# Kernel tuning notes

Measured on AMD Instinct MI355X. Metric: run time of the kernel, lower is better.

Reference implementation:

```python
import jax, jax.numpy as jnp
import numpy as np

# ---- config (mirrors DVE_loss.__init__ defaults used here) ----
POW = 0.5
TEMPERATURE = 1.0
SINK_TAU = 0.3      # sink_tau[1]
SINK_ITERS = 30     # sink_iters[1]
LAMBDA_LC = 1.0
SCALE = 20.0        # F.normalize(...) * 20
EPS = 1e-12


def _l2norm(x, axis):
    n = jnp.sqrt(jnp.sum(x * x, axis=axis, keepdims=True))
    return x / jnp.maximum(n, EPS)


def _sinkhorn(log_alpha, tau, n_iters):
    # log-space Sinkhorn normalization (gumbel_sinkhorn with n_samples=1, no noise)
    la = log_alpha / tau
    def body(i, la):
        la = la - jax.nn.logsumexp(la, axis=1, keepdims=True)  # row normalize
        la = la - jax.nn.logsumexp(la, axis=0, keepdims=True)  # col normalize
        return la
    la = jax.lax.fori_loop(0, n_iters, body, la)
    return jnp.exp(la)


def _per_sample(f1, f2, fa, x1):
    # f1, f2, fa: [N, C] (already normalized * 20); x1: [N, 3]
    N = f1.shape[0]
    dt = f1.dtype

    corr_1a = (f1 @ fa.T) / TEMPERATURE                # [N, N]
    smcorr_1a = jax.nn.softmax(corr_1a, axis=1)
    f1_via_fa_t = smcorr_1a @ fa                        # [N, C] (broadcast-weighted sum)
    corr_1a2 = (f1_via_fa_t @ f2.T) / TEMPERATURE       # [N, N]
    smcorr_1a2 = jax.nn.softmax(corr_1a2, axis=1)

    # no-grad sinkhorn target
    sink = jax.lax.stop_gradient(_sinkhorn(corr_1a2, SINK_TAU, SINK_ITERS))

    # pairwise distance matrix (no-grad): ||xi - xj||^pow
    sq = jnp.sum(x1 * x1, axis=-1)                      # [N]
    d2 = jnp.maximum(sq[:, None] + sq[None, :] - 2.0 * (x1 @ x1.T), 0.0)
    dist = jax.lax.stop_gradient(jnp.sqrt(d2) ** POW)   # [N, N]

    smcorr_12 = jax.nn.softmax((f1 @ f2.T) / TEMPERATURE, axis=1)

    L = dist * smcorr_1a2 + dist * smcorr_12
    loss_b = jnp.sum(L) / N

    perm_to_I_b = 3.0 * jnp.sum(jnp.abs(jnp.eye(N, dtype=dt) - sink)) / N
    Lc_b = 3.0 * jnp.sum(jnp.abs(sink - smcorr_1a2)) / N

    # feature_reconstruction(f1, f1) diagnostic (no-grad)
    g = jax.lax.stop_gradient(f1 @ f1.T)                # [N, N]
    smg = jax.nn.softmax(g / TEMPERATURE, axis=1)
    fv = smg @ jax.lax.stop_gradient(f1)                # [N, C] == (f1 @ smcorr.T).T
    corr2 = fv @ jax.lax.stop_gradient(f1).T            # [N, N] (no temperature div)
    sm2 = jax.nn.softmax(corr2, axis=1)
    d_b = -jnp.sum(jnp.diagonal(sm2)) / N

    match_b = jnp.sum(
        (jnp.argmax(smcorr_1a2, axis=1) == jnp.arange(N)).astype(dt))
    return loss_b, Lc_b, perm_to_I_b, d_b, match_b


def setup_inputs() -> dict:
    key = jax.random.key(0)
    k1, k2 = jax.random.split(key)
    feats = jax.random.normal(k1, (16, 2048, 128), dtype=jnp.float32)
    pc0 = jax.random.normal(k2, (8, 2048, 3), dtype=jnp.float32)
    return {"feats": feats, "pc0": pc0, "epoch": 10}


def reference(feats, pc0, epoch):
    x1 = pc0[..., :3]
    feats1 = feats[0::2]                                # [B, N, C]
    feats2 = feats[1::2]
    B = feats1.shape[0]

    f1 = _l2norm(feats1, axis=-1) * SCALE               # normalize per point
    f2 = _l2norm(feats2, axis=-1) * SCALE
    fa = jnp.roll(f1, -1, axis=0)                       # feats1[(b+1) % B]

    loss_b, Lc_b, perm_b, d_b, match_b = jax.vmap(_per_sample)(f1, f2, fa, x1)

    loss = jnp.sum(loss_b)
    Lc = jnp.sum(Lc_b)
    perm_to_I = jnp.sum(perm_b)
    diff_via_recon = jnp.sum(d_b)
    correct_match = jnp.sum(match_b)

    total_loss = loss + LAMBDA_LC * Lc
    return (total_loss / B, loss / B, Lc / B, perm_to_I / B,
            correct_match / B, diff_via_recon / B)
```

## Files before the change

kernel.cpp:

```cpp
#include <hip/hip_runtime.h>
#include <math.h>

constexpr int B_ = 8;
constexpr int N_ = 2048;
constexpr int D_ = 128;
constexpr long long NDl = (long long)N_ * D_;
constexpr long long NNl = (long long)N_ * N_;
constexpr float INV_TAU = 1.0f / 0.3f;
constexpr float SCALE_ = 20.0f;
constexpr float EPS_ = 1e-12f;

typedef __attribute__((ext_vector_type(8))) short short8;
typedef __attribute__((ext_vector_type(4))) float f32x4;
#define MFMA_BF16 __builtin_amdgcn_mfma_f32_16x16x32_bf16

constexpr size_t FL_F  = (size_t)B_ * NDl;
constexpr size_t FL_NN = (size_t)B_ * NNl;
constexpr size_t FL_V  = (size_t)B_ * N_;

constexpr size_t OFF_SQ   = 0;
constexpr size_t OFF_ROWM = OFF_SQ   + FL_V;
constexpr size_t OFF_ROWZ = OFF_ROWM + FL_V;
constexpr size_t OFF_U0   = OFF_ROWZ + FL_V;
constexpr size_t OFF_V0   = OFF_U0   + FL_V;
constexpr size_t OFF_DIAG = OFF_V0   + FL_V;
constexpr size_t OFF_AV   = OFF_DIAG + FL_V;
constexpr size_t OFF_BV   = OFF_AV   + FL_V;
constexpr size_t OFF_ACC  = OFF_BV   + FL_V;
constexpr size_t OFF_PM   = OFF_ACC  + 16;
constexpr size_t OFF_PS   = OFF_PM   + 32 * FL_V;
constexpr size_t OFF_PT   = OFF_PS   + 32 * FL_V;
constexpr size_t OFF_CP   = OFF_PM;
constexpr size_t OFF_PCM  = OFF_PT;
constexpr size_t OFF_PCS  = OFF_PT + 16 * FL_V;
constexpr size_t OFF_C    = OFF_PM + 128 * FL_V;
constexpr size_t OFF_K    = OFF_C  + FL_NN;
constexpr size_t OFF_BF   = OFF_K  + FL_NN / 2;

__device__ inline float bf2f(unsigned int lo16) {
  return __uint_as_float(lo16 << 16);
}
__device__ inline unsigned int f2bf(float x) {
  unsigned int u = __float_as_uint(x);
  u += 0x7fffu + ((u >> 16) & 1u);
  return (u >> 16) & 0xffffu;
}

__global__ __launch_bounds__(64) void k_norm(const float* __restrict__ feats,
                                             unsigned short* __restrict__ f1hi,
                                             unsigned short* __restrict__ f1lo,
                                             unsigned short* __restrict__ f2hi,
                                             unsigned short* __restrict__ f2lo) {
  int r = blockIdx.x, b = blockIdx.y, which = blockIdx.z;
  const float* src = feats + ((size_t)(2 * b + which)) * NDl + (size_t)r * D_;
  int t = threadIdx.x;
  float2 x = *(const float2*)(src + 2 * t);
  float ss = x.x * x.x + x.y * x.y;
#pragma unroll
  for (int off = 32; off; off >>= 1) ss += __shfl_down(ss, off);
  ss = __shfl(ss, 0);
  float s = SCALE_ / fmaxf(sqrtf(ss), EPS_);
  float y0 = x.x * s, y1 = x.y * s;
  unsigned int h0 = f2bf(y0), h1 = f2bf(y1);
  unsigned int l0 = f2bf(y0 - bf2f(h0)), l1 = f2bf(y1 - bf2f(h1));
  size_t o = (size_t)b * NDl + (size_t)r * D_ + 2 * t;
  unsigned short* hb = (which ? f2hi : f1hi);
  unsigned short* lb = (which ? f2lo : f1lo);
  *(unsigned int*)(hb + o) = h0 | (h1 << 16);
  *(unsigned int*)(lb + o) = l0 | (l1 << 16);
}

__global__ __launch_bounds__(256) void k_transpose(const unsigned short* __restrict__ hi,
                                                   const unsigned short* __restrict__ lo,
                                                   unsigned short* __restrict__ thi,
                                                   unsigned short* __restrict__ tlo) {
  __shared__ unsigned short tile[64][66];
  int rt = blockIdx.x, dt = blockIdx.y, z = blockIdx.z;
  int b = z >> 1;
  const unsigned short* s = ((z & 1) ? lo : hi) + (size_t)b * NDl;
  unsigned short* d = ((z & 1) ? tlo : thi) + (size_t)b * NDl;
  int t = threadIdx.x;
  int r = t >> 2, c0 = (t & 3) * 16;
#pragma unroll
  for (int h = 0; h < 2; ++h) {
    uint4 v = *(const uint4*)(s + (size_t)(rt * 64 + r) * D_ + dt * 64 + c0 + h * 8);
    unsigned short* p = &tile[r][c0 + h * 8];
    p[0] = (unsigned short)v.x; p[1] = (unsigned short)(v.x >> 16);
    p[2] = (unsigned short)v.y; p[3] = (unsigned short)(v.y >> 16);
    p[4] = (unsigned short)v.z; p[5] = (unsigned short)(v.z >> 16);
    p[6] = (unsigned short)v.w; p[7] = (unsigned short)(v.w >> 16);
  }
  __syncthreads();
  int dd = t >> 2, r0 = (t & 3) * 16;
#pragma unroll
  for (int h = 0; h < 2; ++h) {
    unsigned int q[4];
#pragma unroll
    for (int e = 0; e < 4; ++e) {
      unsigned short a0 = tile[r0 + h * 8 + 2 * e][dd];
      unsigned short a1 = tile[r0 + h * 8 + 2 * e + 1][dd];
      q[e] = (unsigned int)a0 | ((unsigned int)a1 << 16);
    }
    uint4 v; v.x = q[0]; v.y = q[1]; v.z = q[2]; v.w = q[3];
    *(uint4*)(d + (size_t)(dt * 64 + dd) * N_ + rt * 64 + r0 + h * 8) = v;
  }
}

__global__ __launch_bounds__(256) void k_sq(const float* __restrict__ pc0,
                                            float* __restrict__ sq) {
  int i = blockIdx.x * 256 + threadIdx.x;
  if (i < B_ * N_) {
    float x = pc0[3 * i], y = pc0[3 * i + 1], z = pc0[3 * i + 2];
    sq[i] = x * x + y * y + z * z;
  }
}

template<bool WRITEC, bool TAU, bool SD, bool DIAG>
__global__ __launch_bounds__(256, 2) void k_mm(
    const unsigned short* __restrict__ Ahi_g, const unsigned short* __restrict__ Alo_g,
    const unsigned short* __restrict__ Bhi_g, const unsigned short* __restrict__ Blo_g,
    float* __restrict__ Cb, int roll,
    float* __restrict__ pms, float* __restrict__ pss, float* __restrict__ pts,
    float* __restrict__ diagb,
    const float* __restrict__ pc0, const float* __restrict__ sqv) {
  int bm = blockIdx.x, bn = blockIdx.y, z = blockIdx.z;
  int zb = (z + roll) & 7;
  const unsigned short* A_hi = Ahi_g + (size_t)z * NDl;
  const unsigned short* A_lo = Alo_g + (size_t)z * NDl;
  const unsigned short* B_hi = Bhi_g + (size_t)zb * NDl;
  const unsigned short* B_lo = Blo_g + (size_t)zb * NDl;
  float* C = Cb + (size_t)z * NNl;

  __shared__ __align__(16) unsigned short sAh[128 * 64], sAl[128 * 64];
  __shared__ __align__(16) unsigned short sBh[128 * 64], sBl[128 * 64];
  __shared__ float rpx[128], rpy[128], rpz[128], rps[128];
  __shared__ float cqx[128], cqy[128], cqz[128], cqs[128];

  int t = threadIdx.x;
  int lane = t & 63, w = t >> 6;
  int wm = w >> 1, wn = w & 1;

  if constexpr (SD) {
    const float* xb = pc0 + (size_t)z * N_ * 3;
    const float* sb = sqv + (size_t)z * N_;
    if (t < 128) {
      int r = bm * 128 + t;
      rpx[t] = xb[3 * r]; rpy[t] = xb[3 * r + 1]; rpz[t] = xb[3 * r + 2]; rps[t] = sb[r];
    } else {
      int c = bn * 128 + (t - 128);
      cqx[t - 128] = xb[3 * c]; cqy[t - 128] = xb[3 * c + 1]; cqz[t - 128] = xb[3 * c + 2];
      cqs[t - 128] = sb[c];
    }
  }

  f32x4 acc[4][4] = {};

  for (int kc = 0; kc < D_; kc += 64) {
    if (kc) __syncthreads();
#pragma unroll
    for (int i = 0; i < 4; ++i) {
      int li = i * 256 + t;
      int r = li >> 3;
      int kb = (li & 7) * 16;
      int sidx = (r * 128 + (kb ^ ((r & 7) << 4))) >> 1;
      size_t ga = (size_t)(bm * 128 + r) * D_ + kc + (kb >> 1);
      size_t gb = (size_t)(bn * 128 + r) * D_ + kc + (kb >> 1);
      *(uint4*)(&sAh[sidx]) = *(const uint4*)(A_hi + ga);
      *(uint4*)(&sAl[sidx]) = *(const uint4*)(A_lo + ga);
      *(uint4*)(&sBh[sidx]) = *(const uint4*)(B_hi + gb);
      *(uint4*)(&sBl[sidx]) = *(const uint4*)(B_lo + gb);
    }
    __syncthreads();

    short8 ah[4][2], al[4][2];
#pragma unroll
    for (int m = 0; m < 4; ++m)
#pragma unroll
      for (int ks = 0; ks < 2; ++ks) {
        int row = wm * 64 + m * 16 + (lane & 15);
        int kb = ks * 64 + ((lane >> 4) * 16);
        int idx = (row * 128 + (kb ^ ((row & 7) << 4))) >> 1;
        ah[m][ks] = *(const short8*)(&sAh[idx]);
        al[m][ks] = *(const short8*)(&sAl[idx]);
      }
#pragma unroll
    for (int n = 0; n < 4; ++n) {
#pragma unroll
      for (int ks = 0; ks < 2; ++ks) {
        int row = wn * 64 + n * 16 + (lane & 15);
        int kb = ks * 64 + ((lane >> 4) * 16);
        int idx = (row * 128 + (kb ^ ((row & 7) << 4))) >> 1;
        short8 bh = *(const short8*)(&sBh[idx]);
        short8 bl = *(const short8*)(&sBl[idx]);
#pragma unroll
        for (int m = 0; m < 4; ++m) {
          acc[m][n] = MFMA_BF16(ah[m][ks], bh, acc[m][n], 0, 0, 0);
          acc[m][n] = MFMA_BF16(ah[m][ks], bl, acc[m][n], 0, 0, 0);
          acc[m][n] = MFMA_BF16(al[m][ks], bh, acc[m][n], 0, 0, 0);
        }
      }
    }
  }

  int lrow = (lane >> 4) * 4;
  int lcol = lane & 15;

  if constexpr (WRITEC) {
#pragma unroll
    for (int m = 0; m < 4; ++m) {
      int gr0 = bm * 128 + wm * 64 + m * 16 + lrow;
#pragma unroll
      for (int n = 0; n < 4; ++n) {
        int gc = bn * 128 + wn * 64 + n * 16 + lcol;
        float* Cp = C + (size_t)gr0 * N_ + gc;
#pragma unroll
        for (int rg = 0; rg < 4; ++rg)
          Cp[(size_t)rg * N_] = acc[m][n][rg];
      }
    }
  }

#pragma unroll
  for (int m = 0; m < 4; ++m) {
#pragma unroll
    for (int rg = 0; rg < 4; ++rg) {
      int rib = wm * 64 + m * 16 + lrow + rg;
      float v0 = acc[m][0][rg], v1 = acc[m][1][rg], v2 = acc[m][2][rg], v3 = acc[m][3][rg];
      float mx = fmaxf(fmaxf(v0, v1), fmaxf(v2, v3));
#pragma unroll
      for (int msk = 1; msk < 16; msk <<= 1) mx = fmaxf(mx, __shfl_xor(mx, msk));
      float e0 = __expf(v0 - mx), e1 = __expf(v1 - mx), e2 = __expf(v2 - mx), e3 = __expf(v3 - mx);
      float s = e0 + e1 + e2 + e3;
      float st = 0.f, sd = 0.f;
      if constexpr (TAU)
        st = __expf((v0 - mx) * INV_TAU) + __expf((v1 - mx) * INV_TAU) +
             __expf((v2 - mx) * INV_TAU) + __expf((v3 - mx) * INV_TAU);
      if constexpr (SD) {
        float xi = rpx[rib], yi = rpy[rib], zi = rpz[rib], si = rps[rib];
#pragma unroll
        for (int n = 0; n < 4; ++n) {
          int ci = wn * 64 + n * 16 + lcol;
          float d2 = fmaxf(si + cqs[ci] - 2.f * (xi * cqx[ci] + yi * cqy[ci] + zi * cqz[ci]), 0.f);
          float en = (n == 0) ? e0 : (n == 1) ? e1 : (n == 2) ? e2 : e3;
          sd += en * sqrtf(sqrtf(d2));
        }
      }
#pragma unroll
      for (int msk = 1; msk < 16; msk <<= 1) {
        s += __shfl_xor(s, msk);
        if constexpr (TAU) st += __shfl_xor(st, msk);
        if constexpr (SD) sd += __shfl_xor(sd, msk);
      }
      if (lcol == 0) {
        size_t idx = ((size_t)(z * 32 + bn * 2 + wn)) * N_ + bm * 128 + rib;
        pms[idx] = mx; pss[idx] = s;
        if constexpr (TAU) pts[idx] = st;
        if constexpr (SD) pts[idx] = sd;
      }
    }
  }

  if constexpr (DIAG) {
    if (bm == bn && wm == wn) {
#pragma unroll
      for (int m = 0; m < 4; ++m)
#pragma unroll
        for (int rg = 0; rg < 4; ++rg) {
          int rr = lrow + rg;
          if (lcol == rr)
            diagb[(size_t)z * N_ + bm * 128 + wm * 64 + m * 16 + rr] = acc[m][m][rg];
        }
    }
  }
}

template<bool WMZ, bool TAU, bool SD, bool DIAG, bool MATCH>
__global__ __launch_bounds__(256) void k_comb(const float* __restrict__ pms,
                                              const float* __restrict__ pss,
                                              const float* __restrict__ pts,
                                              const float* __restrict__ diagb,
                                              float* __restrict__ rowm,
                                              float* __restrict__ rowZ,
                                              float* __restrict__ u0,
                                              float* __restrict__ acc) {
  int b = blockIdx.y;
  int r = blockIdx.x * 256 + threadIdx.x;
  float M = -INFINITY, S = 0.f, ST = 0.f, SDa = 0.f;
#pragma unroll
  for (int p = 0; p < 32; ++p) {
    size_t idx = ((size_t)(b * 32 + p)) * N_ + r;
    float m = pms[idx], s = pss[idx];
    float M2 = fmaxf(M, m);
    float f0 = __expf(M - M2), f1 = __expf(m - M2);
    S = S * f0 + s * f1;
    if constexpr (TAU) ST = ST * __expf((M - M2) * INV_TAU) + pts[idx] * __expf((m - M2) * INV_TAU);
    if constexpr (SD)  SDa = SDa * f0 + pts[idx] * f1;
    M = M2;
  }
  size_t vr = (size_t)b * N_ + r;
  if constexpr (WMZ) { rowm[vr] = M; rowZ[vr] = S; }
  if constexpr (TAU) u0[vr] = M * INV_TAU + __logf(ST);
  float contrib = 0.f; int slot = -1;
  if constexpr (SD)    { contrib = SDa / S; slot = 0; }
  if constexpr (DIAG)  { contrib = __expf(diagb[vr] - M) / S; slot = 3; }
  if constexpr (MATCH) { contrib = (diagb[vr] == M) ? 1.f : 0.f; slot = 4; }
  if (slot >= 0) {
    __shared__ float red[256];
    int t = threadIdx.x;
    red[t] = contrib; __syncthreads();
    for (int off = 128; off; off >>= 1) { if (t < off) red[t] += red[t + off]; __syncthreads(); }
    if (t == 0) atomicAdd(acc + slot, red[0]);
  }
}

__global__ __launch_bounds__(256, 3) void k_smmm(
    const float* __restrict__ Cb, const float* __restrict__ rowm, const float* __restrict__ rowZ,
    const unsigned short* __restrict__ Wthi, const unsigned short* __restrict__ Wtlo,
    unsigned short* __restrict__ Ohi, unsigned short* __restrict__ Olo, int roll) {
  int bm = blockIdx.x, z = blockIdx.y;
  int zb = (z + roll) & 7;
  const float* C = Cb + (size_t)z * NNl + (size_t)(bm * 64) * N_;
  const unsigned short* Wh = Wthi + (size_t)zb * NDl;
  const unsigned short* Wl = Wtlo + (size_t)zb * NDl;

  __shared__ __align__(16) unsigned short sPh[64 * 64], sPl[64 * 64];
  __shared__ __align__(16) unsigned short sWh[128 * 64], sWl[128 * 64];
  __shared__ float s_rm[64], s_rz[64];

  int t = threadIdx.x, lane = t & 63, w = t >> 6;
  if (t < 64) {
    s_rm[t] = rowm[(size_t)z * N_ + bm * 64 + t];
    s_rz[t] = rowZ[(size_t)z * N_ + bm * 64 + t];
  }
  __syncthreads();

  f32x4 acc[8] = {};

  for (int jc = 0; jc < N_; jc += 64) {
    if (jc) __syncthreads();
#pragma unroll
    for (int i = 0; i < 4; ++i) {
      int li = i * 256 + t;
      int r = li >> 4;
      int j4 = (li & 15) * 4;
      float4 c4 = *(const float4*)(C + (size_t)r * N_ + jc + j4);
      float rm = s_rm[r];
      float p0 = __expf(c4.x - rm), p1 = __expf(c4.y - rm);
      float p2 = __expf(c4.z - rm), p3 = __expf(c4.w - rm);
      unsigned int h0 = f2bf(p0), h1 = f2bf(p1), h2 = f2bf(p2), h3 = f2bf(p3);
      unsigned int l0 = f2bf(p0 - bf2f(h0)), l1 = f2bf(p1 - bf2f(h1));
      unsigned int l2 = f2bf(p2 - bf2f(h2)), l3 = f2bf(p3 - bf2f(h3));
      int kb = j4 * 2;
      int sidx = (r * 128 + (kb ^ ((r & 7) << 4))) >> 1;
      uint2 ph; ph.x = h0 | (h1 << 16); ph.y = h2 | (h3 << 16);
      uint2 pl; pl.x = l0 | (l1 << 16); pl.y = l2 | (l3 << 16);
      *(uint2*)(&sPh[sidx]) = ph;
      *(uint2*)(&sPl[sidx]) = pl;
    }
#pragma unroll
    for (int i = 0; i < 4; ++i) {
      int li = i * 256 + t;
      int d = li >> 3;
      int kb = (li & 7) * 16;
      int sidx = (d * 128 + (kb ^ ((d & 7) << 4))) >> 1;
      size_t ga = (size_t)d * N_ + jc + (kb >> 1);
      *(uint4*)(&sWh[sidx]) = *(const uint4*)(Wh + ga);
      *(uint4*)(&sWl[sidx]) = *(const uint4*)(Wl + ga);
    }
    __syncthreads();

    short8 ph[2], pl[2];
#pragma unroll
    for (int ks = 0; ks < 2; ++ks) {
      int row = w * 16 + (lane & 15);
      int kb = ks * 64 + ((lane >> 4) * 16);
      int idx = (row * 128 + (kb ^ ((row & 7) << 4))) >> 1;
      ph[ks] = *(const short8*)(&sPh[idx]);
      pl[ks] = *(const short8*)(&sPl[idx]);
    }
#pragma unroll
    for (int n = 0; n < 8; ++n) {
#pragma unroll
      for (int ks = 0; ks < 2; ++ks) {
        int row = n * 16 + (lane & 15);
        int kb = ks * 64 + ((lane >> 4) * 16);
        int idx = (row * 128 + (kb ^ ((row & 7) << 4))) >> 1;
        short8 bh = *(const short8*)(&sWh[idx]);
        short8 bl = *(const short8*)(&sWl[idx]);
        acc[n] = MFMA_BF16(ph[ks], bh, acc[n], 0, 0, 0);
        acc[n] = MFMA_BF16(ph[ks], bl, acc[n], 0, 0, 0);
        acc[n] = MFMA_BF16(pl[ks], bh, acc[n], 0, 0, 0);
      }
    }
  }

  unsigned short* OhB = Ohi + (size_t)z * NDl;
  unsigned short* OlB = Olo + (size_t)z * NDl;
#pragma unroll
  for (int rg = 0; rg < 4; ++rg) {
    int rib = w * 16 + (lane >> 4) * 4 + rg;
    float iZ = 1.f / s_rz[rib];
    size_t ro = (size_t)(bm * 64 + rib) * D_;
#pragma unroll
    for (int n = 0; n < 8; ++n) {
      int d = n * 16 + (lane & 15);
      float vv = acc[n][rg] * iZ;
      unsigned int h = f2bf(vv);
      OhB[ro + d] = (unsigned short)h;
      OlB[ro + d] = (unsigned short)f2bf(vv - bf2f(h));
    }
  }
}

__global__ __launch_bounds__(256) void k_colLSE(const float* __restrict__ Cb,
                                                const float* __restrict__ u0,
                                                float* __restrict__ pcm,
                                                float* __restrict__ pcs) {
  int jb = blockIdx.x, ch = blockIdx.y, b = blockIdx.z;
  int t = threadIdx.x;
  int j4 = (jb * 256 + t) * 4;
  __shared__ float su[128];
  if (t < 128) su[t] = u0[(size_t)b * N_ + ch * 128 + t];
  __syncthreads();
  const float* Cp = Cb + (size_t)b * NNl + (size_t)(ch * 128) * N_ + j4;
  float m0 = -INFINITY, m1 = -INFINITY, m2 = -INFINITY, m3 = -INFINITY;
  float s0 = 0.f, s1 = 0.f, s2 = 0.f, s3 = 0.f;
#pragma unroll 4
  for (int i = 0; i < 128; ++i) {
    float4 c = *(const float4*)(Cp + (size_t)i * N_);
    float ui = su[i];
    float x0 = c.x * INV_TAU - ui, x1 = c.y * INV_TAU - ui;
    float x2 = c.z * INV_TAU - ui, x3 = c.w * INV_TAU - ui;
    float M0 = fmaxf(m0, x0); s0 = s0 * __expf(m0 - M0) + __expf(x0 - M0); m0 = M0;
    float M1 = fmaxf(m1, x1); s1 = s1 * __expf(m1 - M1) + __expf(x1 - M1); m1 = M1;
    float M2 = fmaxf(m2, x2); s2 = s2 * __expf(m2 - M2) + __expf(x2 - M2); m2 = M2;
    float M3 = fmaxf(m3, x3); s3 = s3 * __expf(m3 - M3) + __expf(x3 - M3); m3 = M3;
  }
  size_t o = ((size_t)(b * 16 + ch)) * N_ + j4;
  float4 vm; vm.x = m0; vm.y = m1; vm.z = m2; vm.w = m3;
  float4 vs; vs.x = s0; vs.y = s1; vs.z = s2; vs.w = s3;
  *(float4*)(pcm + o) = vm;
  *(float4*)(pcs + o) = vs;
}

__global__ __launch_bounds__(256) void k_colLSEcomb(const float* __restrict__ pcm,
                                                    const float* __restrict__ pcs,
                                                    float* __restrict__ v0) {
  int b = blockIdx.y; int j = blockIdx.x * 256 + threadIdx.x;
  float m = -INFINITY, s = 0.f;
#pragma unroll
  for (int ch = 0; ch < 16; ++ch) {
    size_t idx = ((size_t)(b * 16 + ch)) * N_ + j;
    float m2 = pcm[idx], s2 = pcs[idx];
    float M = fmaxf(m, m2);
    s = s * __expf(m - M) + s2 * __expf(m2 - M);
    m = M;
  }
  v0[(size_t)b * N_ + j] = m + __logf(s);
}

template<bool INITK>
__global__ __launch_bounds__(256) void k_sink_iter(const float* __restrict__ Cb,
                                                   unsigned short* __restrict__ Kp,
                                                   const float* __restrict__ u0,
                                                   const float* __restrict__ v0,
                                                   const float* __restrict__ bvec,
                                                   float* __restrict__ avec,
                                                   float* __restrict__ cp) {
  int stripe = blockIdx.x, b = blockIdx.y;
  int i0 = stripe * 16;
  int t = threadIdx.x;
  int w = t >> 6, l = t & 63;
  __shared__ float a_s[16];
  float bv[4][8];
  const float* vsrc = INITK ? (v0 + (size_t)b * N_) : (bvec + (size_t)b * N_);
#pragma unroll
  for (int c = 0; c < 4; ++c) {
    float4 q0 = *(const float4*)(vsrc + c * 512 + l * 8);
    float4 q1 = *(const float4*)(vsrc + c * 512 + l * 8 + 4);
    bv[c][0] = q0.x; bv[c][1] = q0.y; bv[c][2] = q0.z; bv[c][3] = q0.w;
    bv[c][4] = q1.x; bv[c][5] = q1.y; bv[c][6] = q1.z; bv[c][7] = q1.w;
  }
  unsigned short* Kb = Kp + (size_t)b * NNl;
  const float* Cbb = Cb + (size_t)b * NNl;
#pragma unroll
  for (int ii = 0; ii < 4; ++ii) {
    int i = w * 4 + ii;
    int row = i0 + i;
    float r = 0.f;
    if constexpr (INITK) {
      float ub = u0[(size_t)b * N_ + row];
      const float* Crow = Cbb + (size_t)row * N_;
      unsigned short* Krow = Kb + (size_t)row * N_;
#pragma unroll
      for (int c = 0; c < 4; ++c) {
        float4 c0 = *(const float4*)(Crow + c * 512 + l * 8);
        float4 c1 = *(const float4*)(Crow + c * 512 + l * 8 + 4);
        float cv[8] = {c0.x, c0.y, c0.z, c0.w, c1.x, c1.y, c1.z, c1.w};
        float kv[8];
#pragma unroll
        for (int e = 0; e < 8; ++e) { kv[e] = __expf(cv[e] * INV_TAU - ub - bv[c][e]); r += kv[e]; }
        uint4 pk;
        pk.x = f2bf(kv[0]) | (f2bf(kv[1]) << 16);
        pk.y = f2bf(kv[2]) | (f2bf(kv[3]) << 16);
        pk.z = f2bf(kv[4]) | (f2bf(kv[5]) << 16);
        pk.w = f2bf(kv[6]) | (f2bf(kv[7]) << 16);
        *(uint4*)(Krow + c * 512 + l * 8) = pk;
      }
    } else {
      const unsigned short* Krow = Kb + (size_t)row * N_;
      uint4 pk0 = *(const uint4*)(Krow + 0 * 512 + l * 8);
      uint4 pk1 = *(const uint4*)(Krow + 1 * 512 + l * 8);
      uint4 pk2 = *(const uint4*)(Krow + 2 * 512 + l * 8);
      uint4 pk3 = *(const uint4*)(Krow + 3 * 512 + l * 8);
      r += bf2f(pk0.x & 0xffffu) * bv[0][0] + bf2f(pk0.x >> 16) * bv[0][1]
         + bf2f(pk0.y & 0xffffu) * bv[0][2] + bf2f(pk0.y >> 16) * bv[0][3]
         + bf2f(pk0.z & 0xffffu) * bv[0][4] + bf2f(pk0.z >> 16) * bv[0][5]
         + bf2f(pk0.w & 0xffffu) * bv[0][6] + bf2f(pk0.w >> 16) * bv[0][7];
      r += bf2f(pk1.x & 0xffffu) * bv[1][0] + bf2f(pk1.x >> 16) * bv[1][1]
         + bf2f(pk1.y & 0xffffu) * bv[1][2] + bf2f(pk1.y >> 16) * bv[1][3]
         + bf2f(pk1.z & 0xffffu) * bv[1][4] + bf2f(pk1.z >> 16) * bv[1][5]
         + bf2f(pk1.w & 0xffffu) * bv[1][6] + bf2f(pk1.w >> 16) * bv[1][7];
      r += bf2f(pk2.x & 0xffffu) * bv[2][0] + bf2f(pk2.x >> 16) * bv[2][1]
         + bf2f(pk2.y & 0xffffu) * bv[2][2] + bf2f(pk2.y >> 16) * bv[2][3]
         + bf2f(pk2.z & 0xffffu) * bv[2][4] + bf2f(pk2.z >> 16) * bv[2][5]
         + bf2f(pk2.w & 0xffffu) * bv[2][6] + bf2f(pk2.w >> 16) * bv[2][7];
      r += bf2f(pk3.x & 0xffffu) * bv[3][0] + bf2f(pk3.x >> 16) * bv[3][1]
         + bf2f(pk3.y & 0xffffu) * bv[3][2] + bf2f(pk3.y >> 16) * bv[3][3]
         + bf2f(pk3.z & 0xffffu) * bv[3][4] + bf2f(pk3.z >> 16) * bv[3][5]
         + bf2f(pk3.w & 0xffffu) * bv[3][6] + bf2f(pk3.w >> 16) * bv[3][7];
    }
#pragma unroll
    for (int off = 1; off < 64; off <<= 1) r += __shfl_xor(r, off);
    if (l == 0) {
      float a = 1.f / r;
      a_s[i] = a;
      avec[(size_t)b * N_ + row] = a;
    }
  }
  if constexpr (INITK) __threadfence_block();
  __syncthreads();
  float cpa[8] = {};
  const unsigned short* Kc = Kb + (size_t)i0 * N_ + w * 512 + l * 8;
#pragma unroll 4
  for (int i = 0; i < 16; ++i) {
    uint4 pk = *(const uint4*)(Kc + (size_t)i * N_);
    float ai = a_s[i];
    cpa[0] += bf2f(pk.x & 0xffffu) * ai; cpa[1] += bf2f(pk.x >> 16) * ai;
    cpa[2] += bf2f(pk.y & 0xffffu) * ai; cpa[3] += bf2f(pk.y >> 16) * ai;
    cpa[4] += bf2f(pk.z & 0xffffu) * ai; cpa[5] += bf2f(pk.z >> 16) * ai;
    cpa[6] += bf2f(pk.w & 0xffffu) * ai; cpa[7] += bf2f(pk.w >> 16) * ai;
  }
  size_t o = ((size_t)(b * 128 + stripe)) * N_ + w * 512 + l * 8;
  float4 o0; o0.x = cpa[0]; o0.y = cpa[1]; o0.z = cpa[2]; o0.w = cpa[3];
  float4 o1; o1.x = cpa[4]; o1.y = cpa[5]; o1.z = cpa[6]; o1.w = cpa[7];
  *(float4*)(cp + o) = o0;
  *(float4*)(cp + o + 4) = o1;
}

__global__ __launch_bounds__(256) void k_bcomb(const float* __restrict__ cp,
                                               float* __restrict__ bvec) {
  int b = blockIdx.y; int j = blockIdx.x * 256 + threadIdx.x;
  float s0 = 0.f, s1 = 0.f, s2 = 0.f, s3 = 0.f;
#pragma unroll 8
  for (int st = 0; st < 128; st += 4) {
    s0 += cp[((size_t)(b * 128 + st + 0)) * N_ + j];
    s1 += cp[((size_t)(b * 128 + st + 1)) * N_ + j];
    s2 += cp[((size_t)(b * 128 + st + 2)) * N_ + j];
    s3 += cp[((size_t)(b * 128 + st + 3)) * N_ + j];
  }
  bvec[(size_t)b * N_ + j] = 1.f / ((s0 + s1) + (s2 + s3));
}

__global__ __launch_bounds__(256) void k_felem(const float* __restrict__ Cb,
                                               const unsigned short* __restrict__ Kp,
                                               const float* __restrict__ rowm,
                                               const float* __restrict__ rowZ,
                                               const float* __restrict__ avec,
                                               const float* __restrict__ bvec,
                                               const float* __restrict__ pc0,
                                               const float* __restrict__ sqv,
                                               float* __restrict__ acc) {
  int rb = blockIdx.x, b = blockIdx.y;
  int i0 = rb * 16;
  int t = threadIdx.x;
  const float* xb = pc0 + (size_t)b * N_ * 3;
  const float* sqb = sqv + (size_t)b * N_;
  float xj[2][4], yj[2][4], zj[2][4], sj[2][4], bj[2][4];
#pragma unroll
  for (int kk = 0; kk < 2; ++kk) {
    int j4 = t * 4 + kk * 1024;
    float4 p0 = *(const float4*)(xb + 3 * j4);
    float4 p1 = *(const float4*)(xb + 3 * j4 + 4);
    float4 p2 = *(const float4*)(xb + 3 * j4 + 8);
    xj[kk][0] = p0.x; yj[kk][0] = p0.y; zj[kk][0] = p0.z;
    xj[kk][1] = p0.w; yj[kk][1] = p1.x; zj[kk][1] = p1.y;
    xj[kk][2] = p1.z; yj[kk][2] = p1.w; zj[kk][2] = p2.x;
    xj[kk][3] = p2.y; yj[kk][3] = p2.z; zj[kk][3] = p2.w;
    float4 s4 = *(const float4*)(sqb + j4);
    sj[kk][0] = s4.x; sj[kk][1] = s4.y; sj[kk][2] = s4.z; sj[kk][3] = s4.w;
    float4 b4 = *(const float4*)(bvec + (size_t)b * N_ + j4);
    bj[kk][0] = b4.x; bj[kk][1] = b4.y; bj[kk][2] = b4.z; bj[kk][3] = b4.w;
  }
  float aL = 0.f, aLc = 0.f, aP = 0.f;
  for (int ii = 0; ii < 16; ++ii) {
    int i = i0 + ii;
    float xi = xb[3 * i], yi = xb[3 * i + 1], zi = xb[3 * i + 2];
    float sqi = sqb[i];
    float mi = rowm[(size_t)b * N_ + i];
    float iZ = 1.f / rowZ[(size_t)b * N_ + i];
    float ai = avec[(size_t)b * N_ + i];
    const float* Crow = Cb + (size_t)b * NNl + (size_t)i * N_;
    const unsigned short* Krow = Kp + (size_t)b * NNl + (size_t)i * N_;
#pragma unroll
    for (int kk = 0; kk < 2; ++kk) {
      int j4 = t * 4 + kk * 1024;
      float4 c4 = *(const float4*)(Crow + j4);
      uint2 k2 = *(const uint2*)(Krow + j4);
      float kf[4] = { bf2f(k2.x & 0xffffu), bf2f(k2.x >> 16),
                      bf2f(k2.y & 0xffffu), bf2f(k2.y >> 16) };
      float cf[4] = { c4.x, c4.y, c4.z, c4.w };
#pragma unroll
      for (int e = 0; e < 4; ++e) {
        int j = j4 + e;
        float sm = __expf(cf[e] - mi) * iZ;
        float sink = kf[e] * ai * bj[kk][e];
        float d2 = fmaxf(sqi + sj[kk][e] - 2.f * (xi * xj[kk][e] + yi * yj[kk][e] + zi * zj[kk][e]), 0.f);
        aL += sqrtf(sqrtf(d2)) * sm;
        aLc += fabsf(sink - sm);
        aP += fabsf(((i == j) ? 1.f : 0.f) - sink);
      }
    }
  }
  __shared__ float red[256];
  red[t] = aL; __syncthreads();
  for (int off = 128; off; off >>= 1) { if (t < off) red[t] += red[t + off]; __syncthreads(); }
  if (t == 0) atomicAdd(acc + 0, red[0]);
  __syncthreads();
  red[t] = aLc; __syncthreads();
  for (int off = 128; off; off >>= 1) { if (t < off) red[t] += red[t + off]; __syncthreads(); }
  if (t == 0) atomicAdd(acc + 1, red[0]);
  __syncthreads();
  red[t] = aP; __syncthreads();
  for (int off = 128; off; off >>= 1) { if (t < off) red[t] += red[t + off]; __syncthreads(); }
  if (t == 0) atomicAdd(acc + 2, red[0]);
}

__global__ void k_finalize(const float* __restrict__ acc, float* __restrict__ out) {
  float invN = 1.0f / (float)N_;
  float L  = acc[0] * invN;
  float Lc = 3.f * acc[1] * invN;
  float P  = 3.f * acc[2] * invN;
  float Dg = -acc[3] * invN;
  float M  = acc[4];
  float invB = 1.0f / (float)B_;
  out[0] = (L + Lc) * invB;
  out[1] = L * invB;
  out[2] = Lc * invB;
  out[3] = P * invB;
  out[4] = M * invB;
  out[5] = Dg * invB;
}

extern "C" void kernel_launch(void* const* d_in, const int* in_sizes, int n_in,
                              void* d_out, int out_size, void* d_ws, size_t ws_size,
                              hipStream_t stream) {
  const float* feats = (const float*)d_in[0];
  const float* pc0 = (const float*)d_in[1];
  float* out = (float*)d_out;
  float* ws = (float*)d_ws;

  float* sqv   = ws + OFF_SQ;
  float* rowm  = ws + OFF_ROWM;
  float* rowZ  = ws + OFF_ROWZ;
  float* u0    = ws + OFF_U0;
  float* v0    = ws + OFF_V0;
  float* diagb = ws + OFF_DIAG;
  float* avec  = ws + OFF_AV;
  float* bvec  = ws + OFF_BV;
  float* acc   = ws + OFF_ACC;
  float* pms   = ws + OFF_PM;
  float* pss   = ws + OFF_PS;
  float* pts   = ws + OFF_PT;
  float* pcm   = ws + OFF_PCM;
  float* pcs   = ws + OFF_PCS;
  float* cp    = ws + OFF_CP;
  float* C     = ws + OFF_C;
  unsigned short* Kp = (unsigned short*)(ws + OFF_K);
  unsigned short* bfb = (unsigned short*)(ws + OFF_BF);
  unsigned short* f1hi   = bfb + 0 * FL_F;
  unsigned short* f1lo   = bfb + 1 * FL_F;
  unsigned short* f2hi   = bfb + 2 * FL_F;
  unsigned short* f2lo   = bfb + 3 * FL_F;
  unsigned short* f1t_hi = bfb + 4 * FL_F;
  unsigned short* f1t_lo = bfb + 5 * FL_F;
  unsigned short* fvahi  = bfb + 6 * FL_F;
  unsigned short* fvalo  = bfb + 7 * FL_F;

  hipMemsetAsync(acc, 0, 16 * sizeof(float), stream);

  k_norm<<<dim3(N_, B_, 2), 64, 0, stream>>>(feats, f1hi, f1lo, f2hi, f2lo);
  k_transpose<<<dim3(32, 2, 16), 256, 0, stream>>>(f1hi, f1lo, f1t_hi, f1t_lo);
  k_sq<<<(B_ * N_) / 256, 256, 0, stream>>>(pc0, sqv);

  dim3 mmGrid(N_ / 128, N_ / 128, B_);
  dim3 cbGrid(N_ / 256, B_);
  dim3 smGrid(N_ / 64, B_);

  k_mm<true, false, false, false><<<mmGrid, 256, 0, stream>>>(f1hi, f1lo, f1hi, f1lo, C, 0, pms, pss, pts, diagb, pc0, sqv);
  k_comb<true, false, false, false, false><<<cbGrid, 256, 0, stream>>>(pms, pss, pts, diagb, rowm, rowZ, u0, acc);
  k_smmm<<<smGrid, 256, 0, stream>>>(C, rowm, rowZ, f1t_hi, f1t_lo, fvahi, fvalo, 0);
  k_mm<false, false, false, true><<<mmGrid, 256, 0, stream>>>(fvahi, fvalo, f1hi, f1lo, C, 0, pms, pss, pts, diagb, pc0, sqv);
  k_comb<false, false, false, true, false><<<cbGrid, 256, 0, stream>>>(pms, pss, pts, diagb, rowm, rowZ, u0, acc);

  k_mm<false, false, true, false><<<mmGrid, 256, 0, stream>>>(f1hi, f1lo, f2hi, f2lo, C, 0, pms, pss, pts, diagb, pc0, sqv);
  k_comb<false, false, true, false, false><<<cbGrid, 256, 0, stream>>>(pms, pss, pts, diagb, rowm, rowZ, u0, acc);

  k_mm<true, false, false, false><<<mmGrid, 256, 0, stream>>>(f1hi, f1lo, f1hi, f1lo, C, 1, pms, pss, pts, diagb, pc0, sqv);
  k_comb<true, false, false, false, false><<<cbGrid, 256, 0, stream>>>(pms, pss, pts, diagb, rowm, rowZ, u0, acc);
  k_smmm<<<smGrid, 256, 0, stream>>>(C, rowm, rowZ, f1t_hi, f1t_lo, fvahi, fvalo, 1);

  k_mm<true, true, false, true><<<mmGrid, 256, 0, stream>>>(fvahi, fvalo, f2hi, f2lo, C, 0, pms, pss, pts, diagb, pc0, sqv);
  k_comb<true, true, false, false, true><<<cbGrid, 256, 0, stream>>>(pms, pss, pts, diagb, rowm, rowZ, u0, acc);

  k_colLSE<<<dim3(2, 16, B_), 256, 0, stream>>>(C, u0, pcm, pcs);
  k_colLSEcomb<<<cbGrid, 256, 0, stream>>>(pcm, pcs, v0);
  k_sink_iter<true><<<dim3(128, B_), 256, 0, stream>>>(C, Kp, u0, v0, bvec, avec, cp);
  k_bcomb<<<cbGrid, 256, 0, stream>>>(cp, bvec);
  for (int it = 0; it < 28; ++it) {
    k_sink_iter<false><<<dim3(128, B_), 256, 0, stream>>>(C, Kp, u0, v0, bvec, avec, cp);
    k_bcomb<<<cbGrid, 256, 0, stream>>>(cp, bvec);
  }

  k_felem<<<dim3(N_ / 16, B_), 256, 0, stream>>>(C, Kp, rowm, rowZ, avec, bvec, pc0, sqv, acc);

  k_finalize<<<1, 1, 0, stream>>>(acc, out);
}
```

Measured before the change: 1.685 ms.

## Stage GEMM tiles and Sinkhorn K stripes into LDS via direct global-to-LDS loads

Replaces register-staged global-to-shared copies in the GEMM and softmax-matmul kernels with direct global_load_lds transfers, moving the XOR swizzle from the LDS address to the global source address. Splits the Sinkhorn kernel into an init variant and an iteration variant. The iteration variant loads each 16-row bf16 K stripe once into 64KB of LDS and reuses it for both the row-sum and column-partial passes, instead of reading it from global memory twice. The large LDS allocation lowers occupancy, and the swizzle remapping must match the existing read pattern to stay correct.

```diff
diff --git a/kernel.cpp b/kernel.cpp
--- a/kernel.cpp
+++ b/kernel.cpp
@@ -46,6 +46,18 @@
   return (u >> 16) & 0xffffu;
 }
 
+__device__ inline void gload16(const unsigned short* g, unsigned short* lbase, int lane) {
+#if defined(__has_builtin)
+#if __has_builtin(__builtin_amdgcn_global_load_lds)
+  __builtin_amdgcn_global_load_lds(
+      (const __attribute__((address_space(1))) unsigned int*)g,
+      (__attribute__((address_space(3))) unsigned int*)lbase, 16, 0, 0);
+  return;
+#endif
+#endif
+  *(uint4*)(lbase + lane * 8) = *(const uint4*)g;
+}
+
 __global__ __launch_bounds__(64) void k_norm(const float* __restrict__ feats,
                                              unsigned short* __restrict__ f1hi,
                                              unsigned short* __restrict__ f1lo,
@@ -161,14 +173,15 @@
     for (int i = 0; i < 4; ++i) {
       int li = i * 256 + t;
       int r = li >> 3;
-      int kb = (li & 7) * 16;
-      int sidx = (r * 128 + (kb ^ ((r & 7) << 4))) >> 1;
-      size_t ga = (size_t)(bm * 128 + r) * D_ + kc + (kb >> 1);
-      size_t gb = (size_t)(bn * 128 + r) * D_ + kc + (kb >> 1);
-      *(uint4*)(&sAh[sidx]) = *(const uint4*)(A_hi + ga);
-      *(uint4*)(&sAl[sidx]) = *(const uint4*)(A_lo + ga);
-      *(uint4*)(&sBh[sidx]) = *(const uint4*)(B_hi + gb);
-      *(uint4*)(&sBl[sidx]) = *(const uint4*)(B_lo + gb);
+      int j = li & 7;
+      int xoff = (j * 8) ^ ((r & 7) << 3);
+      size_t grow_a = (size_t)(bm * 128 + r) * D_ + kc + xoff;
+      size_t grow_b = (size_t)(bn * 128 + r) * D_ + kc + xoff;
+      int wbase = (i * 256 + (t & 192)) * 8;
+      gload16(A_hi + grow_a, &sAh[wbase], lane);
+      gload16(A_lo + grow_a, &sAl[wbase], lane);
+      gload16(B_hi + grow_b, &sBh[wbase], lane);
+      gload16(B_lo + grow_b, &sBl[wbase], lane);
     }
     __syncthreads();
 
@@ -361,11 +374,12 @@
     for (int i = 0; i < 4; ++i) {
       int li = i * 256 + t;
       int d = li >> 3;
-      int kb = (li & 7) * 16;
-      int sidx = (d * 128 + (kb ^ ((d & 7) << 4))) >> 1;
-      size_t ga = (size_t)d * N_ + jc + (kb >> 1);
-      *(uint4*)(&sWh[sidx]) = *(const uint4*)(Wh + ga);
-      *(uint4*)(&sWl[sidx]) = *(const uint4*)(Wl + ga);
+      int j = li & 7;
+      int xoff = (j * 8) ^ ((d & 7) << 3);
+      size_t ga = (size_t)d * N_ + jc + xoff;
+      int wbase = (i * 256 + (t & 192)) * 8;
+      gload16(Wh + ga, &sWh[wbase], lane);
+      gload16(Wl + ga, &sWl[wbase], lane);
     }
     __syncthreads();
 
@@ -459,12 +473,10 @@
   v0[(size_t)b * N_ + j] = m + __logf(s);
 }
 
-template<bool INITK>
-__global__ __launch_bounds__(256) void k_sink_iter(const float* __restrict__ Cb,
+__global__ __launch_bounds__(256) void k_sink_init(const float* __restrict__ Cb,
                                                    unsigned short* __restrict__ Kp,
                                                    const float* __restrict__ u0,
                                                    const float* __restrict__ v0,
-                                                   const float* __restrict__ bvec,
                                                    float* __restrict__ avec,
                                                    float* __restrict__ cp) {
   int stripe = blockIdx.x, b = blockIdx.y;
@@ -473,7 +485,7 @@
   int w = t >> 6, l = t & 63;
   __shared__ float a_s[16];
   float bv[4][8];
-  const float* vsrc = INITK ? (v0 + (size_t)b * N_) : (bvec + (size_t)b * N_);
+  const float* vsrc = v0 + (size_t)b * N_;
 #pragma unroll
   for (int c = 0; c < 4; ++c) {
     float4 q0 = *(const float4*)(vsrc + c * 512 + l * 8);
@@ -488,47 +500,23 @@
     int i = w * 4 + ii;
     int row = i0 + i;
     float r = 0.f;
-    if constexpr (INITK) {
-      float ub = u0[(size_t)b * N_ + row];
-      const float* Crow = Cbb + (size_t)row * N_;
-      unsigned short* Krow = Kb + (size_t)row * N_;
-#pragma unroll
-      for (int c = 0; c < 4; ++c) {
-        float4 c0 = *(const float4*)(Crow + c * 512 + l * 8);
-        float4 c1 = *(const float4*)(Crow + c * 512 + l * 8 + 4);
-        float cv[8] = {c0.x, c0.y, c0.z, c0.w, c1.x, c1.y, c1.z, c1.w};
-        float kv[8];
-#pragma unroll
-        for (int e = 0; e < 8; ++e) { kv[e] = __expf(cv[e] * INV_TAU - ub - bv[c][e]); r += kv[e]; }
-        uint4 pk;
-        pk.x = f2bf(kv[0]) | (f2bf(kv[1]) << 16);
-        pk.y = f2bf(kv[2]) | (f2bf(kv[3]) << 16);
-        pk.z = f2bf(kv[4]) | (f2bf(kv[5]) << 16);
-        pk.w = f2bf(kv[6]) | (f2bf(kv[7]) << 16);
-        *(uint4*)(Krow + c * 512 + l * 8) = pk;
-      }
-    } else {
-      const unsigned short* Krow = Kb + (size_t)row * N_;
-      uint4 pk0 = *(const uint4*)(Krow + 0 * 512 + l * 8);
-      uint4 pk1 = *(const uint4*)(Krow + 1 * 512 + l * 8);
-      uint4 pk2 = *(const uint4*)(Krow + 2 * 512 + l * 8);
-      uint4 pk3 = *(const uint4*)(Krow + 3 * 512 + l * 8);
-      r += bf2f(pk0.x & 0xffffu) * bv[0][0] + bf2f(pk0.x >> 16) * bv[0][1]
-         + bf2f(pk0.y & 0xffffu) * bv[0][2] + bf2f(pk0.y >> 16) * bv[0][3]
-         + bf2f(pk0.z & 0xffffu) * bv[0][4] + bf2f(pk0.z >> 16) * bv[0][5]
-         + bf2f(pk0.w & 0xffffu) * bv[0][6] + bf2f(pk0.w >> 16) * bv[0][7];
-      r += bf2f(pk1.x & 0xffffu) * bv[1][0] + bf2f(pk1.x >> 16) * bv[1][1]
-         + bf2f(pk1.y & 0xffffu) * bv[1][2] + bf2f(pk1.y >> 16) * bv[1][3]
-         + bf2f(pk1.z & 0xffffu) * bv[1][4] + bf2f(pk1.z >> 16) * bv[1][5]
-         + bf2f(pk1.w & 0xffffu) * bv[1][6] + bf2f(pk1.w >> 16) * bv[1][7];
-      r += bf2f(pk2.x & 0xffffu) * bv[2][0] + bf2f(pk2.x >> 16) * bv[2][1]
-         + bf2f(pk2.y & 0xffffu) * bv[2][2] + bf2f(pk2.y >> 16) * bv[2][3]
-         + bf2f(pk2.z & 0xffffu) * bv[2][4] + bf2f(pk2.z >> 16) * bv[2][5]
-         + bf2f(pk2.w & 0xffffu) * bv[2][6] + bf2f(pk2.w >> 16) * bv[2][7];
-      r += bf2f(pk3.x & 0xffffu) * bv[3][0] + bf2f(pk3.x >> 16) * bv[3][1]
-         + bf2f(pk3.y & 0xffffu) * bv[3][2] + bf2f(pk3.y >> 16) * bv[3][3]
-         + bf2f(pk3.z & 0xffffu) * bv[3][4] + bf2f(pk3.z >> 16) * bv[3][5]
-         + bf2f(pk3.w & 0xffffu) * bv[3][6] + bf2f(pk3.w >> 16) * bv[3][7];
+    float ub = u0[(size_t)b * N_ + row];
+    const float* Crow = Cbb + (size_t)row * N_;
+    unsigned short* Krow = Kb + (size_t)row * N_;
+#pragma unroll
+    for (int c = 0; c < 4; ++c) {
+      float4 c0 = *(const float4*)(Crow + c * 512 + l * 8);
+      float4 c1 = *(const float4*)(Crow + c * 512 + l * 8 + 4);
+      float cv[8] = {c0.x, c0.y, c0.z, c0.w, c1.x, c1.y, c1.z, c1.w};
+      float kv[8];
+#pragma unroll
+      for (int e = 0; e < 8; ++e) { kv[e] = __expf(cv[e] * INV_TAU - ub - bv[c][e]); r += kv[e]; }
+      uint4 pk;
+      pk.x = f2bf(kv[0]) | (f2bf(kv[1]) << 16);
+      pk.y = f2bf(kv[2]) | (f2bf(kv[3]) << 16);
+      pk.z = f2bf(kv[4]) | (f2bf(kv[5]) << 16);
+      pk.w = f2bf(kv[6]) | (f2bf(kv[7]) << 16);
+      *(uint4*)(Krow + c * 512 + l * 8) = pk;
     }
 #pragma unroll
     for (int off = 1; off < 64; off <<= 1) r += __shfl_xor(r, off);
@@ -538,13 +526,80 @@
       avec[(size_t)b * N_ + row] = a;
     }
   }
-  if constexpr (INITK) __threadfence_block();
+  __threadfence_block();
   __syncthreads();
   float cpa[8] = {};
   const unsigned short* Kc = Kb + (size_t)i0 * N_ + w * 512 + l * 8;
 #pragma unroll 4
   for (int i = 0; i < 16; ++i) {
     uint4 pk = *(const uint4*)(Kc + (size_t)i * N_);
+    float ai = a_s[i];
+    cpa[0] += bf2f(pk.x & 0xffffu) * ai; cpa[1] += bf2f(pk.x >> 16) * ai;
+    cpa[2] += bf2f(pk.y & 0xffffu) * ai; cpa[3] += bf2f(pk.y >> 16) * ai;
+    cpa[4] += bf2f(pk.z & 0xffffu) * ai; cpa[5] += bf2f(pk.z >> 16) * ai;
+    cpa[6] += bf2f(pk.w & 0xffffu) * ai; cpa[7] += bf2f(pk.w >> 16) * ai;
+  }
+  size_t o = ((size_t)(b * 128 + stripe)) * N_ + w * 512 + l * 8;
+  float4 o0; o0.x = cpa[0]; o0.y = cpa[1]; o0.z = cpa[2]; o0.w = cpa[3];
+  float4 o1; o1.x = cpa[4]; o1.y = cpa[5]; o1.z = cpa[6]; o1.w = cpa[7];
+  *(float4*)(cp + o) = o0;
+  *(float4*)(cp + o + 4) = o1;
+}
+
+__global__ __launch_bounds__(256) void k_sink_iterL(const unsigned short* __restrict__ Kp,
+                                                    const float* __restrict__ bvec,
+                                                    float* __restrict__ avec,
+                                                    float* __restrict__ cp) {
+  int stripe = blockIdx.x, b = blockIdx.y;
+  int i0 = stripe * 16;
+  int t = threadIdx.x;
+  int w = t >> 6, l = t & 63;
+  __shared__ __align__(16) unsigned short sK[16 * 2048];
+  __shared__ float a_s[16];
+  const unsigned short* Kb = Kp + (size_t)b * NNl + (size_t)i0 * N_;
+#pragma unroll
+  for (int i = 0; i < 16; ++i) {
+    int li = i * 256 + t;
+    int row = li >> 8;
+    int j = li & 255;
+    int wbase = (i * 256 + (t & 192)) * 8;
+    gload16(Kb + (size_t)row * N_ + j * 8, &sK[wbase], l);
+  }
+  float bv[4][8];
+  const float* vsrc = bvec + (size_t)b * N_;
+#pragma unroll
+  for (int c = 0; c < 4; ++c) {
+    float4 q0 = *(const float4*)(vsrc + c * 512 + l * 8);
+    float4 q1 = *(const float4*)(vsrc + c * 512 + l * 8 + 4);
+    bv[c][0] = q0.x; bv[c][1] = q0.y; bv[c][2] = q0.z; bv[c][3] = q0.w;
+    bv[c][4] = q1.x; bv[c][5] = q1.y; bv[c][6] = q1.z; bv[c][7] = q1.w;
+  }
+  __syncthreads();
+#pragma unroll
+  for (int ii = 0; ii < 4; ++ii) {
+    int i = w * 4 + ii;
+    float r = 0.f;
+#pragma unroll
+    for (int c = 0; c < 4; ++c) {
+      uint4 pk = *(const uint4*)(&sK[i * 2048 + c * 512 + l * 8]);
+      r += bf2f(pk.x & 0xffffu) * bv[c][0] + bf2f(pk.x >> 16) * bv[c][1]
+         + bf2f(pk.y & 0xffffu) * bv[c][2] + bf2f(pk.y >> 16) * bv[c][3]
+         + bf2f(pk.z & 0xffffu) * bv[c][4] + bf2f(pk.z >> 16) * bv[c][5]
+         + bf2f(pk.w & 0xffffu) * bv[c][6] + bf2f(pk.w >> 16) * bv[c][7];
+    }
+#pragma unroll
+    for (int off = 1; off < 64; off <<= 1) r += __shfl_xor(r, off);
+    if (l == 0) {
+      float a = 1.f / r;
+      a_s[i] = a;
+      avec[(size_t)b * N_ + i0 + i] = a;
+    }
+  }
+  __syncthreads();
+  float cpa[8] = {};
+#pragma unroll 4
+  for (int i = 0; i < 16; ++i) {
+    uint4 pk = *(const uint4*)(&sK[i * 2048 + w * 512 + l * 8]);
     float ai = a_s[i];
     cpa[0] += bf2f(pk.x & 0xffffu) * ai; cpa[1] += bf2f(pk.x >> 16) * ai;
     cpa[2] += bf2f(pk.y & 0xffffu) * ai; cpa[3] += bf2f(pk.y >> 16) * ai;
@@ -725,10 +780,10 @@
 
   k_colLSE<<<dim3(2, 16, B_), 256, 0, stream>>>(C, u0, pcm, pcs);
   k_colLSEcomb<<<cbGrid, 256, 0, stream>>>(pcm, pcs, v0);
-  k_sink_iter<true><<<dim3(128, B_), 256, 0, stream>>>(C, Kp, u0, v0, bvec, avec, cp);
+  k_sink_init<<<dim3(128, B_), 256, 0, stream>>>(C, Kp, u0, v0, avec, cp);
   k_bcomb<<<cbGrid, 256, 0, stream>>>(cp, bvec);
   for (int it = 0; it < 28; ++it) {
-    k_sink_iter<false><<<dim3(128, B_), 256, 0, stream>>>(C, Kp, u0, v0, bvec, avec, cp);
+    k_sink_iterL<<<dim3(128, B_), 256, 0, stream>>>(Kp, bvec, avec, cp);
     k_bcomb<<<cbGrid, 256, 0, stream>>>(cp, bvec);
   }
 
```

Result: faster. 1.460 ms (-13.4%).
